# Kernel optimization log

Measured on AMD Instinct MI355X. Metric: run time of the kernel, lower is better.

Reference implementation:

```python
import jax, jax.numpy as jnp
import numpy as np

N, E, F_IN, H, F_OUT = 100000, 1600000, 128, 4, 16
NEG_SLOPE = 0.2


def setup_inputs() -> dict:
    key = jax.random.key(0)
    k1, k2, k3, k4, k5 = jax.random.split(key, 5)
    # xavier-ish scales
    s_w = (6.0 / (F_IN + H * F_OUT)) ** 0.5
    s_a = (6.0 / (1 + F_OUT)) ** 0.5
    return {
        "features": jax.random.normal(k1, (N, F_IN), dtype=jnp.float32),
        "edge_index": jax.random.randint(k2, (2, E), 0, N, dtype=jnp.int64),
        "weight_l": jax.random.uniform(k3, (F_IN, H * F_OUT), jnp.float32, -s_w, s_w),
        "weight_r": jax.random.uniform(k4, (F_IN, H * F_OUT), jnp.float32, -s_w, s_w),
        "att": jax.random.uniform(k5, (1, H, F_OUT), jnp.float32, -s_a, s_a),
        "bias": jnp.zeros((H * F_OUT,), dtype=jnp.float32),
    }


def reference(features, edge_index, weight_l, weight_r, att, bias):
    num_nodes = features.shape[0]
    src = edge_index[0]
    tgt = edge_index[1]
    h_l = (features @ weight_l).reshape(-1, H, F_OUT)  # [N,H,F]
    h_r = (features @ weight_r).reshape(-1, H, F_OUT)
    x_i = h_l[tgt]  # [E,H,F] gather target
    x_j = h_r[src]  # [E,H,F] gather source
    z = x_i + x_j
    z = jnp.where(z >= 0, z, NEG_SLOPE * z)  # leaky_relu
    scores = (z * att).sum(axis=-1)  # [E,H]
    # segment softmax keyed by target node
    m = jax.ops.segment_max(scores, tgt, num_segments=num_nodes)  # [N,H]
    ex = jnp.exp(scores - jax.lax.stop_gradient(m)[tgt])
    denom = jax.ops.segment_sum(ex, tgt, num_segments=num_nodes)  # [N,H]
    alpha = ex / denom[tgt]  # [E,H]
    messages = x_j * alpha[..., None]  # [E,H,F]
    out = jax.ops.segment_sum(messages, tgt, num_segments=num_nodes)  # [N,H,F]
    out = out.reshape(num_nodes, H * F_OUT) + bias
    return out
```

## Files before the change

### kernel.cpp

```cpp
#include <hip/hip_runtime.h>

#define NN 100000
#define NE 1600000
#define NB 782
#define CHUNK 4096
#define BCAP 2560
#define LDP 136

typedef __attribute__((ext_vector_type(8))) short bf16x8;
typedef __attribute__((ext_vector_type(4))) float f32x4;

static __device__ __forceinline__ unsigned short f2bf(float f) {
  unsigned int u = __float_as_uint(f);
  u += 0x7fff + ((u >> 16) & 1);
  return (unsigned short)(u >> 16);
}

__global__ void wprep_k(const float* __restrict__ wl, const float* __restrict__ wr,
                        unsigned short* __restrict__ wt, int* __restrict__ bcursor) {
  int i = blockIdx.x * 256 + threadIdx.x;
  int c = i >> 7, k = i & 127;
  float v = (c < 64) ? wl[k * 64 + c] : wr[k * 64 + (c - 64)];
  wt[i] = f2bf(v);
  if (i < NB) bcursor[i * 16] = i * BCAP;
}

__global__ __launch_bounds__(256) void gemm_mfma(const float* __restrict__ feat,
                                                 const unsigned short* __restrict__ wt,
                                                 float* __restrict__ hl,
                                                 unsigned short* __restrict__ hrb) {
  __shared__ unsigned short ldsA[128][LDP];
  const int tid = threadIdx.x;
  const int row0 = blockIdx.x * 128;

  for (int it = 0; it < 16; ++it) {
    int r = it * 8 + (tid >> 5);
    int gr = row0 + r;
    int k4 = (tid & 31) * 4;
    float4 v = make_float4(0.f, 0.f, 0.f, 0.f);
    if (gr < NN) v = *reinterpret_cast<const float4*>(&feat[(size_t)gr * 128 + k4]);
    union { unsigned short s[4]; uint2 u; } pk;
    pk.s[0] = f2bf(v.x); pk.s[1] = f2bf(v.y); pk.s[2] = f2bf(v.z); pk.s[3] = f2bf(v.w);
    *reinterpret_cast<uint2*>(&ldsA[r][k4]) = pk.u;
  }
  __syncthreads();

  const int w  = tid >> 6;
  const int ln = tid & 63;
  const int lr = ln & 15;
  const int kb = (ln >> 4) * 8;

  f32x4 acc[2][8];
#pragma unroll
  for (int mt = 0; mt < 2; ++mt)
#pragma unroll
    for (int nt = 0; nt < 8; ++nt) acc[mt][nt] = (f32x4){0.f, 0.f, 0.f, 0.f};

#pragma unroll
  for (int t = 0; t < 4; ++t) {
    const int ko = t * 32 + kb;
    bf16x8 af0 = *reinterpret_cast<const bf16x8*>(&ldsA[w * 32 + lr][ko]);
    bf16x8 af1 = *reinterpret_cast<const bf16x8*>(&ldsA[w * 32 + 16 + lr][ko]);
    bf16x8 bfr[8];
#pragma unroll
    for (int nt = 0; nt < 8; ++nt)
      bfr[nt] = *reinterpret_cast<const bf16x8*>(&wt[(size_t)(nt * 16 + lr) * 128 + ko]);
#pragma unroll
    for (int nt = 0; nt < 8; ++nt) {
      acc[0][nt] = __builtin_amdgcn_mfma_f32_16x16x32_bf16(af0, bfr[nt], acc[0][nt], 0, 0, 0);
      acc[1][nt] = __builtin_amdgcn_mfma_f32_16x16x32_bf16(af1, bfr[nt], acc[1][nt], 0, 0, 0);
    }
  }

#pragma unroll
  for (int mt = 0; mt < 2; ++mt) {
    int rrel = w * 32 + mt * 16 + (ln >> 4) * 4;
#pragma unroll
    for (int q = 0; q < 4; ++q) {
      int gr = row0 + rrel + q;
      if (gr < NN) {
#pragma unroll
        for (int nt = 0; nt < 4; ++nt)
          hl[(size_t)gr * 64 + nt * 16 + lr] = acc[mt][nt][q];
#pragma unroll
        for (int nt = 4; nt < 8; ++nt)
          hrb[(size_t)gr * 64 + (nt - 4) * 16 + lr] = f2bf(acc[mt][nt][q]);
      }
    }
  }
}

__global__ __launch_bounds__(512) void bscatter_k(const int* __restrict__ edge,
                                                  int* __restrict__ bcursor,
                                                  int* __restrict__ brec) {
  __shared__ int lcnt[NB];
  __shared__ int lstart[NB];
  __shared__ int gbase[NB];
  __shared__ int lcur[NB];
  __shared__ int srec[CHUNK];
  __shared__ unsigned short bid[CHUNK];
  __shared__ int sd[512];
  const int tid = threadIdx.x;
  const int base = blockIdx.x * CHUNK;
  const int lim = min(CHUNK, NE - base);

  for (int b = tid; b < NB; b += 512) { lcnt[b] = 0; lcur[b] = 0; }
  __syncthreads();
  for (int i = tid; i < lim; i += 512)
    atomicAdd(&lcnt[edge[NE + base + i] >> 7], 1);
  __syncthreads();

  int v[2]; int s = 0;
#pragma unroll
  for (int j = 0; j < 2; ++j) {
    int idx = tid * 2 + j;
    v[j] = (idx < NB) ? lcnt[idx] : 0;
    s += v[j];
  }
  sd[tid] = s;
  __syncthreads();
  for (int off = 1; off < 512; off <<= 1) {
    int t = (tid >= off) ? sd[tid - off] : 0;
    __syncthreads();
    sd[tid] += t;
    __syncthreads();
  }
  int run = sd[tid] - s;
#pragma unroll
  for (int j = 0; j < 2; ++j) {
    int idx = tid * 2 + j;
    if (idx < NB) lstart[idx] = run;
    run += v[j];
  }
  __syncthreads();

  for (int b = tid; b < NB; b += 512)
    if (lcnt[b] > 0) gbase[b] = atomicAdd(&bcursor[b * 16], lcnt[b]);
  __syncthreads();

  for (int i = tid; i < lim; i += 512) {
    int tg = edge[NE + base + i];
    int sr = edge[base + i];
    int b = tg >> 7;
    int r = atomicAdd(&lcur[b], 1);
    int slot = lstart[b] + r;
    srec[slot] = (sr << 7) | (tg & 127);
    bid[slot] = (unsigned short)b;
  }
  __syncthreads();

  for (int i = tid; i < lim; i += 512) {
    int b = bid[i];
    brec[gbase[b] + i - lstart[b]] = srec[i];
  }
}

__global__ __launch_bounds__(512) void bsort_k(int* __restrict__ brec,
                                               const int* __restrict__ bcursor,
                                               int2* __restrict__ srange) {
  __shared__ int srec[BCAP];
  __shared__ int ncnt[128];
  __shared__ int nst[128];
  __shared__ int sd2[128];
  const int tid = threadIdx.x;
  const int b = blockIdx.x;
  const int s0 = b * BCAP;
  const int cnt = bcursor[b * 16] - s0;

  if (tid < 128) ncnt[tid] = 0;
  __syncthreads();
  for (int i = tid; i < cnt; i += 512) {
    int r = brec[s0 + i];
    srec[i] = r;
    atomicAdd(&ncnt[r & 127], 1);
  }
  __syncthreads();

  int val = (tid < 128) ? ncnt[tid] : 0;
  if (tid < 128) sd2[tid] = val;
  __syncthreads();
  for (int off = 1; off < 128; off <<= 1) {
    int t = 0;
    if (tid < 128 && tid >= off) t = sd2[tid - off];
    __syncthreads();
    if (tid < 128) sd2[tid] += t;
    __syncthreads();
  }
  if (tid < 128) {
    int st = sd2[tid] - val;
    nst[tid] = st;
    int nid = (b << 7) + tid;
    if (nid < NN) srange[nid] = make_int2(s0 + st, s0 + st + val);
    ncnt[tid] = 0;
  }
  __syncthreads();

  for (int i = tid; i < cnt; i += 512) {
    int r = srec[i];
    int tl = r & 127;
    int p = atomicAdd(&ncnt[tl], 1);
    brec[s0 + nst[tl] + p] = r >> 7;
  }
}

#define UNPK(D_, U0_, U1_)                             \
  D_.x = __uint_as_float((U0_) << 16);                 \
  D_.y = __uint_as_float((U0_) & 0xffff0000u);         \
  D_.z = __uint_as_float((U1_) << 16);                 \
  D_.w = __uint_as_float((U1_) & 0xffff0000u);

#define ACC(AC_, E_, X_)                               \
  AC_.x = fmaf(E_, X_.x, AC_.x); AC_.y = fmaf(E_, X_.y, AC_.y); \
  AC_.z = fmaf(E_, X_.z, AC_.z); AC_.w = fmaf(E_, X_.w, AC_.w);

__global__ __launch_bounds__(256) void node_k(const float* __restrict__ hl,
                                              const unsigned short* __restrict__ hrb,
                                              const int* __restrict__ ssrc,
                                              const int2* __restrict__ srange,
                                              const float* __restrict__ att,
                                              const float* __restrict__ bias,
                                              float* __restrict__ out) {
  const int lane = threadIdx.x & 63;
  const int n  = blockIdx.x * 4 + (threadIdx.x >> 6);
  const int g  = lane >> 4;
  const int fo = (lane & 15) * 4;

  const float4 xi = *reinterpret_cast<const float4*>(hl + (size_t)n * 64 + fo);
  const float4 a  = *reinterpret_cast<const float4*>(att + fo);
  const int2 se = srange[n];
  const int s = se.x, e = se.y;
  const unsigned short* __restrict__ hrp = hrb + fo;

  float  den = 0.f;
  float4 acc = make_float4(0.f, 0.f, 0.f, 0.f);

  for (int i = s; i < e; i += 16) {
    uint2 p[4];
    bool  v[4];
#pragma unroll
    for (int u = 0; u < 4; ++u) {
      int r = i + u * 4 + g;
      v[u] = r < e;
      int j = ssrc[v[u] ? r : s];
      p[u] = *reinterpret_cast<const uint2*>(hrp + (size_t)j * 64);
    }
#pragma unroll
    for (int u = 0; u < 4; ++u) {
      float4 x;
      UNPK(x, p[u].x, p[u].y);
      float4 z;
      z.x = xi.x + x.x; z.y = xi.y + x.y; z.z = xi.z + x.z; z.w = xi.w + x.w;
      z.x = fmaxf(z.x, 0.2f * z.x); z.y = fmaxf(z.y, 0.2f * z.y);
      z.z = fmaxf(z.z, 0.2f * z.z); z.w = fmaxf(z.w, 0.2f * z.w);
      float t = z.x * a.x;
      t = fmaf(z.y, a.y, t); t = fmaf(z.z, a.z, t); t = fmaf(z.w, a.w, t);
      t += __shfl_xor(t, 1); t += __shfl_xor(t, 2);
      float ex = v[u] ? __expf(t) : 0.f;
      den += ex;
      ACC(acc, ex, x);
    }
  }

#pragma unroll
  for (int m = 16; m <= 32; m <<= 1) {
    den   += __shfl_xor(den, m);
    acc.x += __shfl_xor(acc.x, m);
    acc.y += __shfl_xor(acc.y, m);
    acc.z += __shfl_xor(acc.z, m);
    acc.w += __shfl_xor(acc.w, m);
  }

  if (g == 0) {
    float inv = (e > s) ? 1.f / den : 0.f;
    float4 b4 = *reinterpret_cast<const float4*>(bias + fo);
    float4 r;
    r.x = fmaf(acc.x, inv, b4.x);
    r.y = fmaf(acc.y, inv, b4.y);
    r.z = fmaf(acc.z, inv, b4.z);
    r.w = fmaf(acc.w, inv, b4.w);
    *reinterpret_cast<float4*>(out + (size_t)n * 64 + fo) = r;
  }
}

extern "C" void kernel_launch(void* const* d_in, const int* in_sizes, int n_in,
                              void* d_out, int out_size, void* d_ws, size_t ws_size,
                              hipStream_t stream) {
  const float* feat = (const float*)d_in[0];
  const int*   edge = (const int*)d_in[1];
  const float* wl   = (const float*)d_in[2];
  const float* wr   = (const float*)d_in[3];
  const float* att  = (const float*)d_in[4];
  const float* bias = (const float*)d_in[5];
  float* out = (float*)d_out;

  float* hl       = (float*)d_ws;
  unsigned short* hrb = (unsigned short*)(hl + (size_t)NN * 64);
  int*   brec     = (int*)(hrb + (size_t)NN * 64);
  int*   bcursor  = brec + (size_t)NB * BCAP;
  int2*  srange   = (int2*)(bcursor + NB * 16);
  unsigned short* wt = (unsigned short*)(srange + NN);

  const int nchunk = (NE + CHUNK - 1) / CHUNK;
  wprep_k<<<64, 256, 0, stream>>>(wl, wr, wt, bcursor);
  gemm_mfma<<<(NN + 127) / 128, 256, 0, stream>>>(feat, wt, hl, hrb);
  bscatter_k<<<nchunk, 512, 0, stream>>>(edge, bcursor, brec);
  bsort_k<<<NB, 512, 0, stream>>>(brec, bcursor, srange);
  node_k<<<NN / 4, 256, 0, stream>>>(hl, hrb, brec, srange, att, bias, out);
}
```

Before: 214.1 us.

## Store both projections as interleaved bf16 rows and shrink GEMM tile to 64 rows

The GEMM now writes h_l and h_r together into one bf16 buffer of 128 values per node (h_l in the first half, h_r in the second), instead of fp32 h_l plus a separate bf16 h_r. The row tile drops from 128 to 64 per block, which doubles the number of GEMM blocks. The node kernel reads h_l for the target node from the same buffer. This cuts GEMM write traffic and the target-row load, but h_l loses precision by going to bf16, and the source gathers now stride 256 bytes per row instead of 128, which may touch more cache lines.

```diff
diff --git a/kernel.cpp b/kernel.cpp
--- a/kernel.cpp
+++ b/kernel.cpp
@@ -27,13 +27,12 @@
 
 __global__ __launch_bounds__(256) void gemm_mfma(const float* __restrict__ feat,
                                                  const unsigned short* __restrict__ wt,
-                                                 float* __restrict__ hl,
-                                                 unsigned short* __restrict__ hrb) {
-  __shared__ unsigned short ldsA[128][LDP];
+                                                 unsigned short* __restrict__ hb) {
+  __shared__ unsigned short ldsA[64][LDP];
   const int tid = threadIdx.x;
-  const int row0 = blockIdx.x * 128;
-
-  for (int it = 0; it < 16; ++it) {
+  const int row0 = blockIdx.x * 64;
+
+  for (int it = 0; it < 8; ++it) {
     int r = it * 8 + (tid >> 5);
     int gr = row0 + r;
     int k4 = (tid & 31) * 4;
@@ -50,41 +49,32 @@
   const int lr = ln & 15;
   const int kb = (ln >> 4) * 8;
 
-  f32x4 acc[2][8];
-#pragma unroll
-  for (int mt = 0; mt < 2; ++mt)
-#pragma unroll
-    for (int nt = 0; nt < 8; ++nt) acc[mt][nt] = (f32x4){0.f, 0.f, 0.f, 0.f};
+  f32x4 acc[8];
+#pragma unroll
+  for (int nt = 0; nt < 8; ++nt) acc[nt] = (f32x4){0.f, 0.f, 0.f, 0.f};
 
 #pragma unroll
   for (int t = 0; t < 4; ++t) {
     const int ko = t * 32 + kb;
-    bf16x8 af0 = *reinterpret_cast<const bf16x8*>(&ldsA[w * 32 + lr][ko]);
-    bf16x8 af1 = *reinterpret_cast<const bf16x8*>(&ldsA[w * 32 + 16 + lr][ko]);
+    bf16x8 af = *reinterpret_cast<const bf16x8*>(&ldsA[w * 16 + lr][ko]);
     bf16x8 bfr[8];
 #pragma unroll
     for (int nt = 0; nt < 8; ++nt)
       bfr[nt] = *reinterpret_cast<const bf16x8*>(&wt[(size_t)(nt * 16 + lr) * 128 + ko]);
 #pragma unroll
-    for (int nt = 0; nt < 8; ++nt) {
-      acc[0][nt] = __builtin_amdgcn_mfma_f32_16x16x32_bf16(af0, bfr[nt], acc[0][nt], 0, 0, 0);
-      acc[1][nt] = __builtin_amdgcn_mfma_f32_16x16x32_bf16(af1, bfr[nt], acc[1][nt], 0, 0, 0);
-    }
-  }
-
-#pragma unroll
-  for (int mt = 0; mt < 2; ++mt) {
-    int rrel = w * 32 + mt * 16 + (ln >> 4) * 4;
+    for (int nt = 0; nt < 8; ++nt)
+      acc[nt] = __builtin_amdgcn_mfma_f32_16x16x32_bf16(af, bfr[nt], acc[nt], 0, 0, 0);
+  }
+
+  {
+    int rrel = w * 16 + (ln >> 4) * 4;
 #pragma unroll
     for (int q = 0; q < 4; ++q) {
       int gr = row0 + rrel + q;
       if (gr < NN) {
 #pragma unroll
-        for (int nt = 0; nt < 4; ++nt)
-          hl[(size_t)gr * 64 + nt * 16 + lr] = acc[mt][nt][q];
-#pragma unroll
-        for (int nt = 4; nt < 8; ++nt)
-          hrb[(size_t)gr * 64 + (nt - 4) * 16 + lr] = f2bf(acc[mt][nt][q]);
+        for (int nt = 0; nt < 8; ++nt)
+          hb[(size_t)gr * 128 + nt * 16 + lr] = f2bf(acc[nt][q]);
       }
     }
   }
@@ -213,8 +203,7 @@
   AC_.x = fmaf(E_, X_.x, AC_.x); AC_.y = fmaf(E_, X_.y, AC_.y); \
   AC_.z = fmaf(E_, X_.z, AC_.z); AC_.w = fmaf(E_, X_.w, AC_.w);
 
-__global__ __launch_bounds__(256) void node_k(const float* __restrict__ hl,
-                                              const unsigned short* __restrict__ hrb,
+__global__ __launch_bounds__(256) void node_k(const unsigned short* __restrict__ hb,
                                               const int* __restrict__ ssrc,
                                               const int2* __restrict__ srange,
                                               const float* __restrict__ att,
@@ -225,11 +214,13 @@
   const int g  = lane >> 4;
   const int fo = (lane & 15) * 4;
 
-  const float4 xi = *reinterpret_cast<const float4*>(hl + (size_t)n * 64 + fo);
-  const float4 a  = *reinterpret_cast<const float4*>(att + fo);
+  uint2 xiu = *reinterpret_cast<const uint2*>(hb + (size_t)n * 128 + fo);
+  float4 xi;
+  UNPK(xi, xiu.x, xiu.y);
+  const float4 a = *reinterpret_cast<const float4*>(att + fo);
   const int2 se = srange[n];
   const int s = se.x, e = se.y;
-  const unsigned short* __restrict__ hrp = hrb + fo;
+  const unsigned short* __restrict__ hrp = hb + 64 + fo;
 
   float  den = 0.f;
   float4 acc = make_float4(0.f, 0.f, 0.f, 0.f);
@@ -242,7 +233,7 @@
       int r = i + u * 4 + g;
       v[u] = r < e;
       int j = ssrc[v[u] ? r : s];
-      p[u] = *reinterpret_cast<const uint2*>(hrp + (size_t)j * 64);
+      p[u] = *reinterpret_cast<const uint2*>(hrp + (size_t)j * 128);
     }
 #pragma unroll
     for (int u = 0; u < 4; ++u) {
@@ -293,17 +284,16 @@
   const float* bias = (const float*)d_in[5];
   float* out = (float*)d_out;
 
-  float* hl       = (float*)d_ws;
-  unsigned short* hrb = (unsigned short*)(hl + (size_t)NN * 64);
-  int*   brec     = (int*)(hrb + (size_t)NN * 64);
+  unsigned short* hb = (unsigned short*)d_ws;
+  int*   brec     = (int*)(hb + (size_t)NN * 128);
   int*   bcursor  = brec + (size_t)NB * BCAP;
   int2*  srange   = (int2*)(bcursor + NB * 16);
   unsigned short* wt = (unsigned short*)(srange + NN);
 
   const int nchunk = (NE + CHUNK - 1) / CHUNK;
   wprep_k<<<64, 256, 0, stream>>>(wl, wr, wt, bcursor);
-  gemm_mfma<<<(NN + 127) / 128, 256, 0, stream>>>(feat, wt, hl, hrb);
+  gemm_mfma<<<(NN + 63) / 64, 256, 0, stream>>>(feat, wt, hb);
   bscatter_k<<<nchunk, 512, 0, stream>>>(edge, bcursor, brec);
   bsort_k<<<NB, 512, 0, stream>>>(brec, bcursor, srange);
-  node_k<<<NN / 4, 256, 0, stream>>>(hl, hrb, brec, srange, att, bias, out);
-}
+  node_k<<<NN / 4, 256, 0, stream>>>(hb, brec, srange, att, bias, out);
+}
```

New measurement: 228.7 us. 1.07x slower.
